# Optimization experiments

Measured on AMD Instinct MI355X. Metric: run time of the kernel, lower is better.

The kernel has to match this reference:

```python
import jax, jax.numpy as jnp
import numpy as np

N_NODES = 100000
N_EDGES = 1600000
N_FEAT = 64
DIM = 32
N_CLASSES = 10
N_GRAPHS = 64
BN_EPS = 1e-5


def setup_inputs() -> dict:
    key = jax.random.key(0)
    ks = jax.random.split(key, 20)
    x = jax.random.normal(ks[0], (N_NODES, N_FEAT), dtype=jnp.float32)
    edge_index = jax.random.randint(ks[1], (2, N_EDGES), 0, N_NODES, dtype=jnp.int64)
    batch = jnp.sort(jax.random.randint(ks[2], (N_NODES,), 0, N_GRAPHS, dtype=jnp.int64))
    s = 0.1
    # conv1 MLP (in=N_FEAT)
    w1a = jax.random.normal(ks[3], (N_FEAT, DIM), dtype=jnp.float32) * s
    b1a = jnp.zeros((DIM,), jnp.float32)
    w1b = jax.random.normal(ks[4], (DIM, DIM), dtype=jnp.float32) * s
    b1b = jnp.zeros((DIM,), jnp.float32)
    # convs 2-5 MLPs stacked [4, DIM, DIM]
    Wa = jax.random.normal(ks[5], (4, DIM, DIM), dtype=jnp.float32) * s
    Ba = jnp.zeros((4, DIM), jnp.float32)
    Wb = jax.random.normal(ks[6], (4, DIM, DIM), dtype=jnp.float32) * s
    Bb = jnp.zeros((4, DIM), jnp.float32)
    bn_gamma = jnp.ones((5, DIM), jnp.float32)
    bn_beta = jnp.zeros((5, DIM), jnp.float32)
    fc1_w = jax.random.normal(ks[7], (DIM, DIM), dtype=jnp.float32) * s
    fc1_b = jnp.zeros((DIM,), jnp.float32)
    fc2_w = jax.random.normal(ks[8], (DIM, N_CLASSES), dtype=jnp.float32) * s
    fc2_b = jnp.zeros((N_CLASSES,), jnp.float32)
    return dict(x=x, edge_index=edge_index, batch=batch,
                w1a=w1a, b1a=b1a, w1b=w1b, b1b=b1b,
                Wa=Wa, Ba=Ba, Wb=Wb, Bb=Bb,
                bn_gamma=bn_gamma, bn_beta=bn_beta,
                fc1_w=fc1_w, fc1_b=fc1_b, fc2_w=fc2_w, fc2_b=fc2_b)


def _gin_aggr(x, src, dst):
    # sum_{j in N(i)} x_j  + x_i   (eps = 0)
    agg = jax.ops.segment_sum(x[src], dst, num_segments=N_NODES)
    return x + agg


def _mlp(h, wa, ba, wb, bb):
    return jax.nn.relu(h @ wa + ba) @ wb + bb


def _bn(h, gamma, beta):
    mu = jnp.mean(h, axis=0)
    var = jnp.mean((h - mu) ** 2, axis=0)  # biased, torch BN training mode
    return (h - mu) * jax.lax.rsqrt(var + BN_EPS) * gamma + beta


def reference(x, edge_index, batch, w1a, b1a, w1b, b1b, Wa, Ba, Wb, Bb,
              bn_gamma, bn_beta, fc1_w, fc1_b, fc2_w, fc2_b):
    src, dst = edge_index[0], edge_index[1]
    # layer 1 (num_features -> dim)
    h = _mlp(_gin_aggr(x, src, dst), w1a, b1a, w1b, b1b)
    h = _bn(jax.nn.relu(h), bn_gamma[0], bn_beta[0])
    # layers 2-5 (dim -> dim)
    for i in range(4):
        h = _mlp(_gin_aggr(h, src, dst), Wa[i], Ba[i], Wb[i], Bb[i])
        h = _bn(jax.nn.relu(h), bn_gamma[i + 1], bn_beta[i + 1])
    # global add pool over graphs
    g = jax.ops.segment_sum(h, batch, num_segments=N_GRAPHS)  # [G, dim]
    g = jax.nn.relu(g @ fc1_w + fc1_b)
    # dropout: eval mode -> identity
    return g @ fc2_w + fc2_b  # [G, num_classes]
```

## Files before the change

### kernel.cpp

```cpp
#include <hip/hip_runtime.h>
#include <hip/hip_fp16.h>

#define NN 100000
#define NE 1600000
#define NF 64
#define DM 32
#define NG 64
#define NC 10
#define BN_EPS 1e-5f

#define BSHIFT 8
#define NBUCK ((NN + 255) >> 8)
#define CHUNK 8192
#define NCH ((NE + CHUNK - 1) / CHUNK)

__device__ __forceinline__ float2 up2(unsigned u) {
    __half2 h = __builtin_bit_cast(__half2, u);
    return __half22float2(h);
}
__device__ __forceinline__ unsigned pk2(float a, float b) {
    __half2 h = __floats2half2_rn(a, b);
    return __builtin_bit_cast(unsigned, h);
}

__global__ __launch_bounds__(256) void binA_k(const int* __restrict__ ei,
                                              int* __restrict__ bcnt) {
    __shared__ int h[NBUCK];
    for (int i = threadIdx.x; i < NBUCK; i += 256) h[i] = 0;
    __syncthreads();
    long long base = (long long)blockIdx.x * CHUNK;
    int n = (int)((NE - base < CHUNK) ? (NE - base) : CHUNK);
    for (int i = threadIdx.x; i < n; i += 256) {
        int d = ei[NE + base + i];
        atomicAdd(&h[d >> BSHIFT], 1);
    }
    __syncthreads();
    for (int i = threadIdx.x; i < NBUCK; i += 256)
        if (h[i]) atomicAdd(&bcnt[i], h[i]);
}

__global__ __launch_bounds__(512) void binB_k(const int* __restrict__ bcnt,
                                              int* __restrict__ bbase,
                                              int* __restrict__ bcur) {
    __shared__ int s[512];
    int t = threadIdx.x;
    int v = (t < NBUCK) ? bcnt[t] : 0;
    s[t] = v;
    __syncthreads();
    int acc = v;
    for (int off = 1; off < 512; off <<= 1) {
        int add = (t >= off) ? s[t - off] : 0;
        __syncthreads();
        acc += add;
        s[t] = acc;
        __syncthreads();
    }
    if (t < NBUCK) { bbase[t] = acc - v; bcur[t] = acc - v; }
    if (t == 0) bbase[NBUCK] = NE;
}

__global__ __launch_bounds__(256) void binC_k(const int* __restrict__ ei,
                                              int* __restrict__ bcur,
                                              unsigned* __restrict__ binned) {
    __shared__ int cnt[NBUCK];
    __shared__ int ofs[NBUCK];
    __shared__ int idx[NBUCK];
    for (int i = threadIdx.x; i < NBUCK; i += 256) { cnt[i] = 0; idx[i] = 0; }
    __syncthreads();
    long long base = (long long)blockIdx.x * CHUNK;
    int n = (int)((NE - base < CHUNK) ? (NE - base) : CHUNK);
    int d[CHUNK / 256];
#pragma unroll
    for (int k = 0; k < CHUNK / 256; k++) {
        int i = threadIdx.x + k * 256;
        int dd = (i < n) ? ei[NE + base + i] : -1;
        d[k] = dd;
        if (dd >= 0) atomicAdd(&cnt[dd >> BSHIFT], 1);
    }
    __syncthreads();
    for (int i = threadIdx.x; i < NBUCK; i += 256)
        if (cnt[i]) ofs[i] = atomicAdd(&bcur[i], cnt[i]);
    __syncthreads();
#pragma unroll
    for (int k = 0; k < CHUNK / 256; k++) {
        int i = threadIdx.x + k * 256;
        if (i < n) {
            unsigned src = (unsigned)ei[base + i];
            int b = d[k] >> BSHIFT;
            int l = atomicAdd(&idx[b], 1);
            binned[ofs[b] + l] = (src << 8) | (unsigned)(d[k] & 255);
        }
    }
}

__global__ __launch_bounds__(256) void binD_k(const unsigned* __restrict__ binned,
                                              const int* __restrict__ bbase,
                                              int* __restrict__ rowptr,
                                              int* __restrict__ csr) {
    __shared__ int cnt[256];
    __shared__ int cur[256];
    __shared__ int s[256];
    int b = blockIdx.x;
    int e0 = bbase[b], e1 = bbase[b + 1];
    int t = threadIdx.x;
    cnt[t] = 0;
    __syncthreads();
    for (int e = e0 + t; e < e1; e += 256) atomicAdd(&cnt[binned[e] & 255u], 1);
    __syncthreads();
    int v = cnt[t];
    s[t] = v;
    __syncthreads();
    int acc = v;
    for (int off = 1; off < 256; off <<= 1) {
        int add = (t >= off) ? s[t - off] : 0;
        __syncthreads();
        acc += add;
        s[t] = acc;
        __syncthreads();
    }
    int base = e0 + acc - v;
    int node = (b << BSHIFT) + t;
    if (node < NN) rowptr[node] = base;
    cur[t] = base;
    if (b == NBUCK - 1 && t == 0) rowptr[NN] = NE;
    __syncthreads();
    for (int e = e0 + t; e < e1; e += 256) {
        unsigned w = binned[e];
        int p = atomicAdd(&cur[w & 255u], 1);
        csr[p] = (int)(w >> 8);
    }
}

__global__ __launch_bounds__(256) void pre1_k(const float* __restrict__ x,
                                              const float* __restrict__ wa,
                                              float* __restrict__ y,
                                              unsigned* __restrict__ yhf,
                                              float* __restrict__ zbuf) {
    __shared__ float sWa[64 * 32];
    int tid = threadIdx.x;
    if (blockIdx.x == 0) {
        for (int i = tid; i < 5 * 64 + NG * 32; i += 256) zbuf[i] = 0.f;
    }
    for (int i = tid; i < 64 * 32; i += 256) sWa[i] = wa[i];
    __syncthreads();
    int l = tid & 3;
    int node = blockIdx.x * 64 + (tid >> 2);
    if (node >= NN) return;
    float t[8];
#pragma unroll
    for (int j = 0; j < 8; j++) t[j] = 0.f;
    const float4* xr = reinterpret_cast<const float4*>(x + (long long)node * 64);
    const float4* w4 = reinterpret_cast<const float4*>(sWa);
#pragma unroll
    for (int k4 = 0; k4 < 16; k4++) {
        float4 xv = xr[k4];
        float av[4] = {xv.x, xv.y, xv.z, xv.w};
#pragma unroll
        for (int i = 0; i < 4; i++) {
            float a = av[i];
            float4 w0 = w4[(k4 * 4 + i) * 8 + 2 * l];
            float4 w1 = w4[(k4 * 4 + i) * 8 + 2 * l + 1];
            t[0] += a * w0.x; t[1] += a * w0.y; t[2] += a * w0.z; t[3] += a * w0.w;
            t[4] += a * w1.x; t[5] += a * w1.y; t[6] += a * w1.z; t[7] += a * w1.w;
        }
    }
    float4* yr = reinterpret_cast<float4*>(y + (long long)node * 32 + l * 8);
    float4 o0, o1;
    o0.x = t[0]; o0.y = t[1]; o0.z = t[2]; o0.w = t[3];
    o1.x = t[4]; o1.y = t[5]; o1.z = t[6]; o1.w = t[7];
    yr[0] = o0; yr[1] = o1;
    uint4 p;
    p.x = pk2(t[0], t[1]); p.y = pk2(t[2], t[3]);
    p.z = pk2(t[4], t[5]); p.w = pk2(t[6], t[7]);
    reinterpret_cast<uint4*>(yhf)[(long long)node * 4 + l] = p;
}

#define SSTR 65
template <int MODE>
__global__ __launch_bounds__(256) void fused_k(const float* __restrict__ selfRow,
                                               float* __restrict__ hOut,
                                               const unsigned* __restrict__ tblIn,
                                               unsigned* __restrict__ tblOut,
                                               const int* __restrict__ rowptr,
                                               const int* __restrict__ csr,
                                               const float* __restrict__ wa,
                                               const float* __restrict__ ba,
                                               const float* __restrict__ wb,
                                               const float* __restrict__ bb,
                                               const float* __restrict__ stPrev,
                                               const float* __restrict__ gammaPrev,
                                               const float* __restrict__ betaPrev,
                                               float* __restrict__ statsOut) {
    __shared__ float sWa[32 * 32];
    __shared__ float sWb[32 * 32];
    __shared__ float sBa[32], sBb[32];
    __shared__ float sSc[32], sSh[32];
    __shared__ float sStage[32 * SSTR];
    __shared__ float sSum[4 * 32], sSq[4 * 32];
    int tid = threadIdx.x;
    for (int i = tid; i < 32 * 32; i += 256) {
        sWb[i] = wb[i];
        if (MODE) sWa[i] = wa[i];
    }
    if (tid < 32) {
        sBa[tid] = ba[tid];
        sBb[tid] = bb[tid];
        if (MODE) {
            const float invn = 1.0f / NN;
            float mu = stPrev[tid] * invn;
            float var = stPrev[32 + tid] * invn - mu * mu;
            float scale = rsqrtf(var + BN_EPS) * gammaPrev[tid];
            sSc[tid] = scale;
            sSh[tid] = betaPrev[tid] - mu * scale;
        }
    }

    int l = tid & 3;
    int nl = tid >> 2;
    int node = blockIdx.x * 64 + nl;
    bool act = node < NN;

    int s = 0, e = 0;
    if (act) { s = rowptr[node]; e = rowptr[node + 1]; }
    const uint4* t4 = reinterpret_cast<const uint4*>(tblIn);
    float g[8];
#pragma unroll
    for (int c = 0; c < 8; c++) g[c] = 0.f;
    int i = s;
    for (; i + 4 <= e; i += 4) {
        int s0 = csr[i], s1 = csr[i + 1], s2 = csr[i + 2], s3 = csr[i + 3];
        uint4 w0 = t4[(long long)s0 * 4 + l];
        uint4 w1 = t4[(long long)s1 * 4 + l];
        uint4 w2 = t4[(long long)s2 * 4 + l];
        uint4 w3 = t4[(long long)s3 * 4 + l];
        float2 p;
        p = up2(w0.x); g[0] += p.x; g[1] += p.y;
        p = up2(w0.y); g[2] += p.x; g[3] += p.y;
        p = up2(w0.z); g[4] += p.x; g[5] += p.y;
        p = up2(w0.w); g[6] += p.x; g[7] += p.y;
        p = up2(w1.x); g[0] += p.x; g[1] += p.y;
        p = up2(w1.y); g[2] += p.x; g[3] += p.y;
        p = up2(w1.z); g[4] += p.x; g[5] += p.y;
        p = up2(w1.w); g[6] += p.x; g[7] += p.y;
        p = up2(w2.x); g[0] += p.x; g[1] += p.y;
        p = up2(w2.y); g[2] += p.x; g[3] += p.y;
        p = up2(w2.z); g[4] += p.x; g[5] += p.y;
        p = up2(w2.w); g[6] += p.x; g[7] += p.y;
        p = up2(w3.x); g[0] += p.x; g[1] += p.y;
        p = up2(w3.y); g[2] += p.x; g[3] += p.y;
        p = up2(w3.z); g[4] += p.x; g[5] += p.y;
        p = up2(w3.w); g[6] += p.x; g[7] += p.y;
    }
    for (; i < e; i++) {
        uint4 w = t4[(long long)csr[i] * 4 + l];
        float2 p;
        p = up2(w.x); g[0] += p.x; g[1] += p.y;
        p = up2(w.y); g[2] += p.x; g[3] += p.y;
        p = up2(w.z); g[4] += p.x; g[5] += p.y;
        p = up2(w.w); g[6] += p.x; g[7] += p.y;
    }
    __syncthreads();

    float t[8];
    if (MODE) {
        float in[8];
        if (act) {
            const float4* hr = reinterpret_cast<const float4*>(selfRow + (long long)node * 32 + l * 8);
            float4 h0 = hr[0], h1 = hr[1];
            float deg = (float)(e - s);
            float hv[8] = {h0.x, h0.y, h0.z, h0.w, h1.x, h1.y, h1.z, h1.w};
#pragma unroll
            for (int c = 0; c < 8; c++) {
                int f = l * 8 + c;
                in[c] = hv[c] * sSc[f] + sSh[f] + (g[c] * sSc[f] + deg * sSh[f]);
            }
        } else {
#pragma unroll
            for (int c = 0; c < 8; c++) in[c] = 0.f;
        }
#pragma unroll
        for (int c = 0; c < 8; c++) sStage[(l * 8 + c) * SSTR + nl] = in[c];
        __syncthreads();
#pragma unroll
        for (int j = 0; j < 8; j++) t[j] = sBa[l * 8 + j];
        const float4* w4a = reinterpret_cast<const float4*>(sWa);
#pragma unroll
        for (int k = 0; k < 32; k++) {
            float a = sStage[k * SSTR + nl];
            float4 w0 = w4a[k * 8 + 2 * l];
            float4 w1 = w4a[k * 8 + 2 * l + 1];
            t[0] += a * w0.x; t[1] += a * w0.y; t[2] += a * w0.z; t[3] += a * w0.w;
            t[4] += a * w1.x; t[5] += a * w1.y; t[6] += a * w1.z; t[7] += a * w1.w;
        }
#pragma unroll
        for (int j = 0; j < 8; j++) t[j] = fmaxf(t[j], 0.f);
        __syncthreads();
    } else {
        if (act) {
            const float4* yr = reinterpret_cast<const float4*>(selfRow + (long long)node * 32 + l * 8);
            float4 y0 = yr[0], y1 = yr[1];
            float yv[8] = {y0.x, y0.y, y0.z, y0.w, y1.x, y1.y, y1.z, y1.w};
#pragma unroll
            for (int c = 0; c < 8; c++) t[c] = fmaxf(yv[c] + g[c] + sBa[l * 8 + c], 0.f);
        } else {
#pragma unroll
            for (int c = 0; c < 8; c++) t[c] = 0.f;
        }
    }

#pragma unroll
    for (int c = 0; c < 8; c++) sStage[(l * 8 + c) * SSTR + nl] = t[c];
    __syncthreads();
    float r[8];
#pragma unroll
    for (int j = 0; j < 8; j++) r[j] = sBb[l * 8 + j];
    const float4* w4b = reinterpret_cast<const float4*>(sWb);
#pragma unroll
    for (int k = 0; k < 32; k++) {
        float a = sStage[k * SSTR + nl];
        float4 w0 = w4b[k * 8 + 2 * l];
        float4 w1 = w4b[k * 8 + 2 * l + 1];
        r[0] += a * w0.x; r[1] += a * w0.y; r[2] += a * w0.z; r[3] += a * w0.w;
        r[4] += a * w1.x; r[5] += a * w1.y; r[6] += a * w1.z; r[7] += a * w1.w;
    }
#pragma unroll
    for (int j = 0; j < 8; j++) r[j] = fmaxf(r[j], 0.f);

    if (act) {
        float4* orow = reinterpret_cast<float4*>(hOut + (long long)node * 32 + l * 8);
        float4 o0, o1;
        o0.x = r[0]; o0.y = r[1]; o0.z = r[2]; o0.w = r[3];
        o1.x = r[4]; o1.y = r[5]; o1.z = r[6]; o1.w = r[7];
        orow[0] = o0; orow[1] = o1;
        uint4 p;
        p.x = pk2(r[0], r[1]); p.y = pk2(r[2], r[3]);
        p.z = pk2(r[4], r[5]); p.w = pk2(r[6], r[7]);
        reinterpret_cast<uint4*>(tblOut)[(long long)node * 4 + l] = p;
    } else {
#pragma unroll
        for (int j = 0; j < 8; j++) r[j] = 0.f;
    }

    int lane = tid & 63, wid = tid >> 6;
#pragma unroll
    for (int j = 0; j < 8; j++) {
        float v = r[j], v2 = v * v;
        v += __shfl_down(v, 32, 64); v2 += __shfl_down(v2, 32, 64);
        v += __shfl_down(v, 16, 64); v2 += __shfl_down(v2, 16, 64);
        v += __shfl_down(v, 8, 64);  v2 += __shfl_down(v2, 8, 64);
        v += __shfl_down(v, 4, 64);  v2 += __shfl_down(v2, 4, 64);
        if (lane < 4) { sSum[wid * 32 + lane * 8 + j] = v; sSq[wid * 32 + lane * 8 + j] = v2; }
    }
    __syncthreads();
    if (tid < 32) {
        float a = sSum[tid] + sSum[32 + tid] + sSum[64 + tid] + sSum[96 + tid];
        float b = sSq[tid] + sSq[32 + tid] + sSq[64 + tid] + sSq[96 + tid];
        atomicAdd(&statsOut[tid], a);
        atomicAdd(&statsOut[32 + tid], b);
    }
}

#define POOL_NPB 512
__global__ __launch_bounds__(256) void pool_bn_k(const float* __restrict__ h,
                                                 const int* __restrict__ batch,
                                                 const float* __restrict__ st,
                                                 const float* __restrict__ gamma,
                                                 const float* __restrict__ beta,
                                                 float* __restrict__ pooled) {
    int tid = threadIdx.x;
    int f = tid & 31;
    int p = tid >> 5;
    int n0 = blockIdx.x * POOL_NPB + p * (POOL_NPB / 8);
    int n1 = n0 + POOL_NPB / 8;
    if (n1 > NN) n1 = NN;
    if (n0 >= NN) return;
    const float invn = 1.0f / NN;
    float mu = st[f] * invn;
    float var = st[32 + f] * invn - mu * mu;
    float sc = rsqrtf(var + BN_EPS) * gamma[f];
    float sh = beta[f] - mu * sc;
    float acc = 0.f;
    int cur = batch[n0];
    for (int n = n0; n < n1; n++) {
        int g = batch[n];
        if (g != cur) {
            atomicAdd(&pooled[cur * 32 + f], acc);
            cur = g;
            acc = 0.f;
        }
        acc += h[(long long)n * 32 + f] * sc + sh;
    }
    atomicAdd(&pooled[cur * 32 + f], acc);
}

__global__ __launch_bounds__(64) void final_k(const float* __restrict__ pooled,
                                              const float* __restrict__ w1,
                                              const float* __restrict__ b1,
                                              const float* __restrict__ w2,
                                              const float* __restrict__ b2,
                                              float* __restrict__ out) {
    int g = threadIdx.x;
    if (g >= NG) return;
    float t[32];
#pragma unroll
    for (int j = 0; j < 32; j++) t[j] = b1[j];
    for (int k = 0; k < 32; k++) {
        float a = pooled[g * 32 + k];
#pragma unroll
        for (int j = 0; j < 32; j++) t[j] += a * w1[k * 32 + j];
    }
#pragma unroll
    for (int j = 0; j < 32; j++) t[j] = fmaxf(t[j], 0.f);
    for (int c = 0; c < NC; c++) {
        float o = b2[c];
#pragma unroll
        for (int k = 0; k < 32; k++) o += t[k] * w2[k * NC + c];
        out[g * NC + c] = o;
    }
}

extern "C" void kernel_launch(void* const* d_in, const int* in_sizes, int n_in,
                              void* d_out, int out_size, void* d_ws, size_t ws_size,
                              hipStream_t stream) {
    const float* x = (const float*)d_in[0];
    const int* ei = (const int*)d_in[1];
    const int* batch = (const int*)d_in[2];
    const float* w1a = (const float*)d_in[3];
    const float* b1a = (const float*)d_in[4];
    const float* w1b = (const float*)d_in[5];
    const float* b1b = (const float*)d_in[6];
    const float* Wa = (const float*)d_in[7];
    const float* Ba = (const float*)d_in[8];
    const float* Wb = (const float*)d_in[9];
    const float* Bb = (const float*)d_in[10];
    const float* bn_gamma = (const float*)d_in[11];
    const float* bn_beta = (const float*)d_in[12];
    const float* fc1w = (const float*)d_in[13];
    const float* fc1b = (const float*)d_in[14];
    const float* fc2w = (const float*)d_in[15];
    const float* fc2b = (const float*)d_in[16];
    float* out = (float*)d_out;

    float* ws = (float*)d_ws;
    float* y = ws;
    float* hb = y + (size_t)NN * 32;
    float* stats_all = hb + (size_t)NN * 32;
    float* pooled = stats_all + 5 * 64;
    unsigned* yhf = (unsigned*)(pooled + NG * 32);
    unsigned* hfA = yhf + (size_t)NN * 16;
    unsigned* hfB = hfA + (size_t)NN * 16;
    unsigned* binned = hfB + (size_t)NN * 16;
    int* bcnt = (int*)(binned + NE);
    int* bbase = bcnt + NBUCK;
    int* bcur = bbase + NBUCK + 1;
    int* rowptr = bcur + NBUCK;
    int* csr = rowptr + NN + 1;

    const int nb4 = (NN + 63) / 64;

    hipMemsetAsync(bcnt, 0, NBUCK * sizeof(int), stream);
    binA_k<<<NCH, 256, 0, stream>>>(ei, bcnt);
    binB_k<<<1, 512, 0, stream>>>(bcnt, bbase, bcur);
    binC_k<<<NCH, 256, 0, stream>>>(ei, bcur, binned);
    binD_k<<<NBUCK, 256, 0, stream>>>(binned, bbase, rowptr, csr);

    pre1_k<<<nb4, 256, 0, stream>>>(x, w1a, y, yhf, stats_all);
    fused_k<0><<<nb4, 256, 0, stream>>>(y, hb, yhf, hfA, rowptr, csr,
                                        nullptr, b1a, w1b, b1b,
                                        nullptr, nullptr, nullptr, stats_all);

    unsigned* tin = hfA;
    unsigned* tout = hfB;
    for (int i = 0; i < 4; i++) {
        fused_k<1><<<nb4, 256, 0, stream>>>(hb, hb, tin, tout, rowptr, csr,
                                            Wa + i * 1024, Ba + i * 32,
                                            Wb + i * 1024, Bb + i * 32,
                                            stats_all + i * 64, bn_gamma + i * 32,
                                            bn_beta + i * 32, stats_all + (i + 1) * 64);
        unsigned* tmp = tin; tin = tout; tout = tmp;
    }

    pool_bn_k<<<(NN + POOL_NPB - 1) / POOL_NPB, 256, 0, stream>>>(
        hb, batch, stats_all + 4 * 64, bn_gamma + 4 * 32, bn_beta + 4 * 32, pooled);
    final_k<<<1, 64, 0, stream>>>(pooled, fc1w, fc1b, fc2w, fc2b, out);
}
```

Before: 528.3 us.

## Drop fp32 activation copies and read self rows from fp16 table

```diff
diff --git a/kernel.cpp b/kernel.cpp
--- a/kernel.cpp
+++ b/kernel.cpp
@@ -21,6 +21,13 @@
 __device__ __forceinline__ unsigned pk2(float a, float b) {
     __half2 h = __floats2half2_rn(a, b);
     return __builtin_bit_cast(unsigned, h);
+}
+__device__ __forceinline__ void acc8(float* a, uint4 w) {
+    float2 p;
+    p = up2(w.x); a[0] += p.x; a[1] += p.y;
+    p = up2(w.y); a[2] += p.x; a[3] += p.y;
+    p = up2(w.z); a[4] += p.x; a[5] += p.y;
+    p = up2(w.w); a[6] += p.x; a[7] += p.y;
 }
 
 __global__ __launch_bounds__(256) void binA_k(const int* __restrict__ ei,
@@ -133,7 +140,6 @@
 
 __global__ __launch_bounds__(256) void pre1_k(const float* __restrict__ x,
                                               const float* __restrict__ wa,
-                                              float* __restrict__ y,
                                               unsigned* __restrict__ yhf,
                                               float* __restrict__ zbuf) {
     __shared__ float sWa[64 * 32];
@@ -164,11 +170,6 @@
             t[4] += a * w1.x; t[5] += a * w1.y; t[6] += a * w1.z; t[7] += a * w1.w;
         }
     }
-    float4* yr = reinterpret_cast<float4*>(y + (long long)node * 32 + l * 8);
-    float4 o0, o1;
-    o0.x = t[0]; o0.y = t[1]; o0.z = t[2]; o0.w = t[3];
-    o1.x = t[4]; o1.y = t[5]; o1.z = t[6]; o1.w = t[7];
-    yr[0] = o0; yr[1] = o1;
     uint4 p;
     p.x = pk2(t[0], t[1]); p.y = pk2(t[2], t[3]);
     p.z = pk2(t[4], t[5]); p.w = pk2(t[6], t[7]);
@@ -177,9 +178,7 @@
 
 #define SSTR 65
 template <int MODE>
-__global__ __launch_bounds__(256) void fused_k(const float* __restrict__ selfRow,
-                                               float* __restrict__ hOut,
-                                               const unsigned* __restrict__ tblIn,
+__global__ __launch_bounds__(256) void fused_k(const unsigned* __restrict__ tblIn,
                                                unsigned* __restrict__ tblOut,
                                                const int* __restrict__ rowptr,
                                                const int* __restrict__ csr,
@@ -221,58 +220,63 @@
     bool act = node < NN;
 
     int s = 0, e = 0;
-    if (act) { s = rowptr[node]; e = rowptr[node + 1]; }
+    uint4 selfw = make_uint4(0, 0, 0, 0);
     const uint4* t4 = reinterpret_cast<const uint4*>(tblIn);
+    if (act) {
+        s = rowptr[node];
+        e = rowptr[node + 1];
+        selfw = t4[(long long)node * 4 + l];
+    }
     float g[8];
 #pragma unroll
     for (int c = 0; c < 8; c++) g[c] = 0.f;
     int i = s;
-    for (; i + 4 <= e; i += 4) {
+    for (; i + 8 <= e; i += 8) {
+        int s0 = csr[i], s1 = csr[i + 1], s2 = csr[i + 2], s3 = csr[i + 3];
+        int s4 = csr[i + 4], s5 = csr[i + 5], s6 = csr[i + 6], s7 = csr[i + 7];
+        uint4 w0 = t4[(long long)s0 * 4 + l];
+        uint4 w1 = t4[(long long)s1 * 4 + l];
+        uint4 w2 = t4[(long long)s2 * 4 + l];
+        uint4 w3 = t4[(long long)s3 * 4 + l];
+        uint4 w4 = t4[(long long)s4 * 4 + l];
+        uint4 w5 = t4[(long long)s5 * 4 + l];
+        uint4 w6 = t4[(long long)s6 * 4 + l];
+        uint4 w7 = t4[(long long)s7 * 4 + l];
+        acc8(g, w0); acc8(g, w1); acc8(g, w2); acc8(g, w3);
+        acc8(g, w4); acc8(g, w5); acc8(g, w6); acc8(g, w7);
+    }
+    if (i + 4 <= e) {
         int s0 = csr[i], s1 = csr[i + 1], s2 = csr[i + 2], s3 = csr[i + 3];
         uint4 w0 = t4[(long long)s0 * 4 + l];
         uint4 w1 = t4[(long long)s1 * 4 + l];
         uint4 w2 = t4[(long long)s2 * 4 + l];
         uint4 w3 = t4[(long long)s3 * 4 + l];
-        float2 p;
-        p = up2(w0.x); g[0] += p.x; g[1] += p.y;
-        p = up2(w0.y); g[2] += p.x; g[3] += p.y;
-        p = up2(w0.z); g[4] += p.x; g[5] += p.y;
-        p = up2(w0.w); g[6] += p.x; g[7] += p.y;
-        p = up2(w1.x); g[0] += p.x; g[1] += p.y;
-        p = up2(w1.y); g[2] += p.x; g[3] += p.y;
-        p = up2(w1.z); g[4] += p.x; g[5] += p.y;
-        p = up2(w1.w); g[6] += p.x; g[7] += p.y;
-        p = up2(w2.x); g[0] += p.x; g[1] += p.y;
-        p = up2(w2.y); g[2] += p.x; g[3] += p.y;
-        p = up2(w2.z); g[4] += p.x; g[5] += p.y;
-        p = up2(w2.w); g[6] += p.x; g[7] += p.y;
-        p = up2(w3.x); g[0] += p.x; g[1] += p.y;
-        p = up2(w3.y); g[2] += p.x; g[3] += p.y;
-        p = up2(w3.z); g[4] += p.x; g[5] += p.y;
-        p = up2(w3.w); g[6] += p.x; g[7] += p.y;
+        acc8(g, w0); acc8(g, w1); acc8(g, w2); acc8(g, w3);
+        i += 4;
     }
     for (; i < e; i++) {
         uint4 w = t4[(long long)csr[i] * 4 + l];
+        acc8(g, w);
+    }
+    __syncthreads();
+
+    float sv[8];
+    {
         float2 p;
-        p = up2(w.x); g[0] += p.x; g[1] += p.y;
-        p = up2(w.y); g[2] += p.x; g[3] += p.y;
-        p = up2(w.z); g[4] += p.x; g[5] += p.y;
-        p = up2(w.w); g[6] += p.x; g[7] += p.y;
-    }
-    __syncthreads();
-
+        p = up2(selfw.x); sv[0] = p.x; sv[1] = p.y;
+        p = up2(selfw.y); sv[2] = p.x; sv[3] = p.y;
+        p = up2(selfw.z); sv[4] = p.x; sv[5] = p.y;
+        p = up2(selfw.w); sv[6] = p.x; sv[7] = p.y;
+    }
     float t[8];
     if (MODE) {
         float in[8];
         if (act) {
-            const float4* hr = reinterpret_cast<const float4*>(selfRow + (long long)node * 32 + l * 8);
-            float4 h0 = hr[0], h1 = hr[1];
             float deg = (float)(e - s);
-            float hv[8] = {h0.x, h0.y, h0.z, h0.w, h1.x, h1.y, h1.z, h1.w};
 #pragma unroll
             for (int c = 0; c < 8; c++) {
                 int f = l * 8 + c;
-                in[c] = hv[c] * sSc[f] + sSh[f] + (g[c] * sSc[f] + deg * sSh[f]);
+                in[c] = sv[c] * sSc[f] + sSh[f] + (g[c] * sSc[f] + deg * sSh[f]);
             }
         } else {
 #pragma unroll
@@ -297,11 +301,8 @@
         __syncthreads();
     } else {
         if (act) {
-            const float4* yr = reinterpret_cast<const float4*>(selfRow + (long long)node * 32 + l * 8);
-            float4 y0 = yr[0], y1 = yr[1];
-            float yv[8] = {y0.x, y0.y, y0.z, y0.w, y1.x, y1.y, y1.z, y1.w};
-#pragma unroll
-            for (int c = 0; c < 8; c++) t[c] = fmaxf(yv[c] + g[c] + sBa[l * 8 + c], 0.f);
+#pragma unroll
+            for (int c = 0; c < 8; c++) t[c] = fmaxf(sv[c] + g[c] + sBa[l * 8 + c], 0.f);
         } else {
 #pragma unroll
             for (int c = 0; c < 8; c++) t[c] = 0.f;
@@ -327,11 +328,6 @@
     for (int j = 0; j < 8; j++) r[j] = fmaxf(r[j], 0.f);
 
     if (act) {
-        float4* orow = reinterpret_cast<float4*>(hOut + (long long)node * 32 + l * 8);
-        float4 o0, o1;
-        o0.x = r[0]; o0.y = r[1]; o0.z = r[2]; o0.w = r[3];
-        o1.x = r[4]; o1.y = r[5]; o1.z = r[6]; o1.w = r[7];
-        orow[0] = o0; orow[1] = o1;
         uint4 p;
         p.x = pk2(r[0], r[1]); p.y = pk2(r[2], r[3]);
         p.z = pk2(r[4], r[5]); p.w = pk2(r[6], r[7]);
@@ -361,7 +357,7 @@
 }
 
 #define POOL_NPB 512
-__global__ __launch_bounds__(256) void pool_bn_k(const float* __restrict__ h,
+__global__ __launch_bounds__(256) void pool_bn_k(const unsigned* __restrict__ tbl,
                                                  const int* __restrict__ batch,
                                                  const float* __restrict__ st,
                                                  const float* __restrict__ gamma,
@@ -370,6 +366,8 @@
     int tid = threadIdx.x;
     int f = tid & 31;
     int p = tid >> 5;
+    int wrd = f >> 1;
+    int hi = f & 1;
     int n0 = blockIdx.x * POOL_NPB + p * (POOL_NPB / 8);
     int n1 = n0 + POOL_NPB / 8;
     if (n1 > NN) n1 = NN;
@@ -388,7 +386,8 @@
             cur = g;
             acc = 0.f;
         }
-        acc += h[(long long)n * 32 + f] * sc + sh;
+        float2 pv = up2(tbl[(long long)n * 16 + wrd]);
+        acc += (hi ? pv.y : pv.x) * sc + sh;
     }
     atomicAdd(&pooled[cur * 32 + f], acc);
 }
@@ -442,9 +441,7 @@
     float* out = (float*)d_out;
 
     float* ws = (float*)d_ws;
-    float* y = ws;
-    float* hb = y + (size_t)NN * 32;
-    float* stats_all = hb + (size_t)NN * 32;
+    float* stats_all = ws;
     float* pooled = stats_all + 5 * 64;
     unsigned* yhf = (unsigned*)(pooled + NG * 32);
     unsigned* hfA = yhf + (size_t)NN * 16;
@@ -464,15 +461,15 @@
     binC_k<<<NCH, 256, 0, stream>>>(ei, bcur, binned);
     binD_k<<<NBUCK, 256, 0, stream>>>(binned, bbase, rowptr, csr);
 
-    pre1_k<<<nb4, 256, 0, stream>>>(x, w1a, y, yhf, stats_all);
-    fused_k<0><<<nb4, 256, 0, stream>>>(y, hb, yhf, hfA, rowptr, csr,
+    pre1_k<<<nb4, 256, 0, stream>>>(x, w1a, yhf, stats_all);
+    fused_k<0><<<nb4, 256, 0, stream>>>(yhf, hfA, rowptr, csr,
                                         nullptr, b1a, w1b, b1b,
                                         nullptr, nullptr, nullptr, stats_all);
 
     unsigned* tin = hfA;
     unsigned* tout = hfB;
     for (int i = 0; i < 4; i++) {
-        fused_k<1><<<nb4, 256, 0, stream>>>(hb, hb, tin, tout, rowptr, csr,
+        fused_k<1><<<nb4, 256, 0, stream>>>(tin, tout, rowptr, csr,
                                             Wa + i * 1024, Ba + i * 32,
                                             Wb + i * 1024, Bb + i * 32,
                                             stats_all + i * 64, bn_gamma + i * 32,
@@ -481,6 +478,6 @@
     }
 
     pool_bn_k<<<(NN + POOL_NPB - 1) / POOL_NPB, 256, 0, stream>>>(
-        hb, batch, stats_all + 4 * 64, bn_gamma + 4 * 32, bn_beta + 4 * 32, pooled);
+        tin, batch, stats_all + 4 * 64, bn_gamma + 4 * 32, bn_beta + 4 * 32, pooled);
     final_k<<<1, 64, 0, stream>>>(pooled, fc1w, fc1b, fc2w, fc2b, out);
 }
```

Result: faster. 499.6 us (-5.4%).
